# Performance work log

Hardware: AMD Instinct MI355X
Metric: run time of the kernel (lower is better)

Reference implementation:

```python
import jax, jax.numpy as jnp
import numpy as np

B, SQ, D = 4, 2048, 1536
HEADS, KV_HEADS, HEAD_DIM = 24, 12, 64
CROSS_DIM = 768
TEXT_LEN, NUM_TOKENS = 512, 64
ENC_LEN = TEXT_LEN + NUM_TOKENS
ROT_DIM = 32
IP_SCALE = 1.0
SCALE = 1.0 / np.sqrt(HEAD_DIM).astype(np.float32)


def _split_heads(x, n_heads):
    # [B, S, n_heads*HEAD_DIM] -> [B, n_heads, S, HEAD_DIM]
    b, s, _ = x.shape
    return x.reshape(b, s, n_heads, HEAD_DIM).transpose(0, 2, 1, 3)


def _repeat_kv(x):
    # [B, KV_HEADS, S, D] -> [B, HEADS, S, D] (repeat_interleave on head dim)
    return jnp.repeat(x, HEADS // KV_HEADS, axis=1)


def _apply_rope(x, cos, sin):
    # x: [B, H, S, ROT_DIM]; cos/sin: [S, ROT_DIM]; use_real_unbind_dim=-2 convention
    xr = x.reshape(*x.shape[:-1], 2, ROT_DIM // 2)
    x_real, x_imag = xr[..., 0, :], xr[..., 1, :]
    x_rot = jnp.concatenate([-x_imag, x_real], axis=-1)
    return x * cos[None, None] + x_rot * sin[None, None]


def _attn(q, k, v):
    scores = jnp.einsum('bhqd,bhkd->bhqk', q, k) * SCALE
    probs = jax.nn.softmax(scores.astype(jnp.float32), axis=-1).astype(q.dtype)
    return jnp.einsum('bhqk,bhkd->bhqd', probs, v)


def setup_inputs():
    key = jax.random.key(0)
    ks = jax.random.split(key, 10)
    t = jnp.arange(SQ, dtype=jnp.float32)
    freqs = 1.0 / (10000.0 ** (jnp.arange(ROT_DIM // 2, dtype=jnp.float32) / (ROT_DIM // 2)))
    ang = t[:, None] * freqs[None, :]  # [SQ, ROT_DIM//2]
    rope_cos = jnp.concatenate([jnp.cos(ang), jnp.cos(ang)], axis=-1)
    rope_sin = jnp.concatenate([jnp.sin(ang), jnp.sin(ang)], axis=-1)
    s = 0.02
    return {
        'hidden_states': jax.random.normal(ks[0], (B, SQ, D), jnp.float32),
        'encoder_hidden_states': jax.random.normal(ks[1], (B, ENC_LEN, CROSS_DIM), jnp.float32),
        'rope_cos': rope_cos,
        'rope_sin': rope_sin,
        'wq': jax.random.normal(ks[2], (D, HEADS * HEAD_DIM), jnp.float32) * s,
        'wk': jax.random.normal(ks[3], (CROSS_DIM, KV_HEADS * HEAD_DIM), jnp.float32) * s,
        'wv': jax.random.normal(ks[4], (CROSS_DIM, KV_HEADS * HEAD_DIM), jnp.float32) * s,
        'wk_ip': jax.random.normal(ks[5], (CROSS_DIM, KV_HEADS * HEAD_DIM), jnp.float32) * s,
        'wv_ip': jax.random.normal(ks[6], (CROSS_DIM, KV_HEADS * HEAD_DIM), jnp.float32) * s,
        'wo': jax.random.normal(ks[7], (HEADS * HEAD_DIM, D), jnp.float32) * s,
        'bo': jnp.zeros((D,), jnp.float32),
    }


def reference(hidden_states, encoder_hidden_states, rope_cos, rope_sin,
              wq, wk, wv, wk_ip, wv_ip, wo, bo):
    residual = hidden_states
    text = encoder_hidden_states[:, :TEXT_LEN, :]
    ip = encoder_hidden_states[:, TEXT_LEN:, :]

    q = _split_heads(hidden_states @ wq, HEADS)          # [B, H, SQ, Dh]
    k = _repeat_kv(_split_heads(text @ wk, KV_HEADS))    # [B, H, St, Dh]
    v = _repeat_kv(_split_heads(text @ wv, KV_HEADS))

    # RoPE in float32 on first ROT_DIM channels of Q only (cross-attention)
    q32 = q.astype(jnp.float32)
    q_rot = _apply_rope(q32[..., :ROT_DIM], rope_cos, rope_sin)
    q = jnp.concatenate([q_rot, q32[..., ROT_DIM:]], axis=-1).astype(hidden_states.dtype)

    out = _attn(q, k, v)                                 # [B, H, SQ, Dh]

    # IP-adapter branch
    ip_k = _repeat_kv(_split_heads(ip @ wk_ip, KV_HEADS))  # [B, H, NUM_TOKENS, Dh]
    ip_v = _repeat_kv(_split_heads(ip @ wv_ip, KV_HEADS))
    out = out + IP_SCALE * _attn(q, ip_k, ip_v)

    out = out.transpose(0, 2, 1, 3).reshape(B, SQ, HEADS * HEAD_DIM)
    out = out @ wo + bo
    return out + residual
```

## Files before the change

kernel.cpp:

```cpp
#include <hip/hip_runtime.h>
#include <hip/hip_bf16.h>

typedef __attribute__((ext_vector_type(8))) short short8;
typedef __attribute__((ext_vector_type(4))) short short4v;
typedef __attribute__((ext_vector_type(4))) float f32x4;

#define MFMA16(a, b, c) __builtin_amdgcn_mfma_f32_16x16x32_bf16(a, b, c, 0, 0, 0)
#define QK_SCALE_LOG2E 0.18033688011112042f

__device__ __forceinline__ short f2bf(float x) {
  union { float f; unsigned u; } v; v.f = x;
  unsigned u = v.u;
  u += 0x7FFFu + ((u >> 16) & 1u);
  return (short)(u >> 16);
}
__device__ __forceinline__ short f2bf_trunc(float x) {
  union { float f; unsigned u; } v; v.f = x;
  return (short)(v.u >> 16);
}

__device__ __forceinline__ void gload16(const void* g, void* l) {
  __builtin_amdgcn_global_load_lds(
      (const __attribute__((address_space(1))) unsigned int*)g,
      (__attribute__((address_space(3))) unsigned int*)l, 16, 0, 0);
}

__global__ __launch_bounds__(256) void conv_bf16_kernel(
    const float* __restrict__ in, short* __restrict__ out, int n4) {
  int i = blockIdx.x * 256 + threadIdx.x;
  if (i >= n4) return;
  f32x4 v = *(const f32x4*)(in + (size_t)i * 4);
  short4v s;
  s[0] = f2bf(v[0]); s[1] = f2bf(v[1]); s[2] = f2bf(v[2]); s[3] = f2bf(v[3]);
  *(short4v*)(out + (size_t)i * 4) = s;
}

__global__ __launch_bounds__(256) void enc_pack_kernel(
    const float* __restrict__ enc, short* __restrict__ text,
    short* __restrict__ ip) {
  int i4 = blockIdx.x * 256 + threadIdx.x;
  int i = i4 * 4;
  if (i >= 4 * 576 * 768) return;
  int c = i % 768;
  int rs = i / 768;
  int b = rs / 576, s = rs % 576;
  f32x4 v = *(const f32x4*)(enc + i);
  short4v o;
  o[0] = f2bf(v[0]); o[1] = f2bf(v[1]); o[2] = f2bf(v[2]); o[3] = f2bf(v[3]);
  if (s < 512)
    *(short4v*)(text + (size_t)(b * 512 + s) * 768 + c) = o;
  else
    *(short4v*)(ip + (size_t)(b * 64 + (s - 512)) * 768 + c) = o;
}

__global__ __launch_bounds__(256) void prep_weights_kernel(
    const float* __restrict__ wq, const float* __restrict__ wo,
    const float* __restrict__ wk, const float* __restrict__ wv,
    const float* __restrict__ wkip, const float* __restrict__ wvip,
    short* __restrict__ wqT, short* __restrict__ woT,
    short* __restrict__ wkvT, short* __restrict__ wkvipT) {
  __shared__ float tile[32][33];
  const int z = blockIdx.z;
  const float* src; short* dst; int N, row_off;
  if (z == 0)      { src = wq;   dst = wqT;    N = 1536; row_off = 0; }
  else if (z == 1) { src = wo;   dst = woT;    N = 1536; row_off = 0; }
  else if (z == 2) { src = wk;   dst = wkvT;   N = 768;  row_off = 0; }
  else if (z == 3) { src = wv;   dst = wkvT;   N = 768;  row_off = 768; }
  else if (z == 4) { src = wkip; dst = wkvipT; N = 768;  row_off = 0; }
  else             { src = wvip; dst = wkvipT; N = 768;  row_off = 768; }
  int c0 = blockIdx.x * 32, r0 = blockIdx.y * 32;
  if (c0 >= N || r0 >= N) return;
  int tx = threadIdx.x & 31, ty = threadIdx.x >> 5;
#pragma unroll
  for (int j = 0; j < 4; ++j)
    tile[ty + j * 8][tx] = src[(size_t)(r0 + ty + j * 8) * N + c0 + tx];
  __syncthreads();
#pragma unroll
  for (int j = 0; j < 4; ++j)
    dst[(size_t)(row_off + c0 + ty + j * 8) * N + r0 + tx] =
        f2bf(tile[tx][ty + j * 8]);
}

__device__ __forceinline__ void gemm_core(
    const short* __restrict__ A, const short* __restrict__ Bt, int K, int lda,
    int ldb, int row0, int col0, short* sA, short* sB, f32x4 acc[4][4]) {
  const int tid = threadIdx.x;
  const int lane = tid & 63;
  const int wid = tid >> 6;
  const int wr = (wid >> 1) * 64, wc = (wid & 1) * 64;
  const int lr = lane & 15;
  const int hk = (lane >> 4) * 16;
  const int xr = (lr & 7) << 4;

  for (int kt = 0; kt < K; kt += 64) {
#pragma unroll
    for (int q = 0; q < 4; ++q) {
      int L = q * 4096 + tid * 16;
      int r = L >> 7;
      int sb = (L & 127) ^ ((r & 7) << 4);
      int srcoff = kt + (sb >> 1);
      gload16(A + (size_t)(row0 + r) * lda + srcoff, (char*)sA + L);
      gload16(Bt + (size_t)(col0 + r) * ldb + srcoff, (char*)sB + L);
    }
    __syncthreads();
#pragma unroll
    for (int kk = 0; kk < 2; ++kk) {
      short8 af[4], bf[4];
#pragma unroll
      for (int m = 0; m < 4; ++m) {
        int row = wr + m * 16 + lr;
        af[m] = *(const short8*)((const char*)sA + row * 128 +
                                 ((kk * 64 + hk) ^ xr));
      }
#pragma unroll
      for (int n = 0; n < 4; ++n) {
        int row = wc + n * 16 + lr;
        bf[n] = *(const short8*)((const char*)sB + row * 128 +
                                 ((kk * 64 + hk) ^ xr));
      }
#pragma unroll
      for (int m = 0; m < 4; ++m)
#pragma unroll
        for (int n = 0; n < 4; ++n) acc[m][n] = MFMA16(af[m], bf[n], acc[m][n]);
    }
    __syncthreads();
  }
}

__device__ __forceinline__ void stage32(const short* __restrict__ gA,
                                        const short* __restrict__ gBt,
                                        int lda, int ldb, char* buf, int tid) {
#pragma unroll
  for (int li = 0; li < 2; ++li) {
    int L = li * 4096 + tid * 16;
    int row = L >> 6;
    int cb = (L & 63) ^ (((row >> 1) & 3) << 4);
    gload16(gA + (size_t)row * lda + (cb >> 1), buf + L);
    gload16(gBt + (size_t)row * ldb + (cb >> 1), buf + 8192 + L);
  }
}

template <int K>
__device__ __forceinline__ void gemm128p(
    const short* __restrict__ A, const short* __restrict__ Bt, int lda,
    int ldb, int row0, int col0, char* sm, f32x4 acc[4][4]) {
  const int tid = threadIdx.x;
  const int lane = tid & 63, wid = tid >> 6;
  const int wr = (wid >> 1) * 64, wc = (wid & 1) * 64;
  const int lr = lane & 15;
  const int hk = (lane >> 4) * 16;
  const int xr = ((lr >> 1) & 3) << 4;
  constexpr int NT = K / 32;

  const short* gA = A + (size_t)row0 * lda;
  const short* gB = Bt + (size_t)col0 * ldb;

  char* p0 = sm;
  char* p1 = sm + 16384;
  char* p2 = sm + 32768;

  stage32(gA, gB, lda, ldb, p0, tid);
  stage32(gA + 32, gB + 32, lda, ldb, p1, tid);
  asm volatile("s_waitcnt vmcnt(4)" ::: "memory");
  __builtin_amdgcn_s_barrier();

  for (int t = 0; t < NT; ++t) {
    if (t + 2 < NT)
      stage32(gA + (t + 2) * 32, gB + (t + 2) * 32, lda, ldb, p2, tid);
    __builtin_amdgcn_sched_barrier(0);
    short8 af[4], bf[4];
#pragma unroll
    for (int m = 0; m < 4; ++m) {
      int row = wr + m * 16 + lr;
      af[m] = *(const short8*)(p0 + row * 64 + (hk ^ xr));
    }
#pragma unroll
    for (int n = 0; n < 4; ++n) {
      int row = wc + n * 16 + lr;
      bf[n] = *(const short8*)(p0 + 8192 + row * 64 + (hk ^ xr));
    }
#pragma unroll
    for (int m = 0; m < 4; ++m)
#pragma unroll
      for (int n = 0; n < 4; ++n) acc[m][n] = MFMA16(af[m], bf[n], acc[m][n]);
    __builtin_amdgcn_sched_barrier(0);
    if (t + 2 < NT)
      asm volatile("s_waitcnt vmcnt(4)" ::: "memory");
    else
      asm volatile("s_waitcnt vmcnt(0)" ::: "memory");
    __builtin_amdgcn_s_barrier();
    char* tmp = p0; p0 = p1; p1 = p2; p2 = tmp;
  }
}

__device__ __forceinline__ void grid128(int& row0, int& col0) {
  int bid = blockIdx.x;
  int x = bid & 7;
  int j = bid >> 3;
  row0 = (x * 8 + (j & 7)) * 128;
  col0 = (j >> 3) * 128;
}

__global__ __launch_bounds__(256, 3) void q_proj_128p(
    const short* __restrict__ hsbf, const short* __restrict__ wqT,
    const float* __restrict__ rc, const float* __restrict__ rsn,
    short* __restrict__ qbuf) {
  __shared__ char sm[49152];
  f32x4 acc[4][4] = {};
  int row0, col0;
  grid128(row0, col0);
  gemm128p<1536>(hsbf, wqT, 1536, 1536, row0, col0, sm, acc);

  const int lane = threadIdx.x & 63, wid = threadIdx.x >> 6;
  const int wr = (wid >> 1) * 64, wc = (wid & 1) * 64;
  const int lr = lane & 15, lrow4 = (lane >> 4) * 4;
  const int h = (col0 + wc) >> 6;
#pragma unroll
  for (int m = 0; m < 4; ++m) {
#pragma unroll
    for (int r = 0; r < 4; ++r) {
      int grow = row0 + wr + m * 16 + lrow4 + r;
      int b = grow >> 11, t = grow & 2047;
      float v0 = acc[m][0][r], v1 = acc[m][1][r];
      float c0 = rc[t * 32 + lr], s0 = rsn[t * 32 + lr];
      float c1 = rc[t * 32 + 16 + lr], s1 = rsn[t * 32 + 16 + lr];
      float n0 = (v0 * c0 - v1 * s0) * QK_SCALE_LOG2E;
      float n1 = (v1 * c1 + v0 * s1) * QK_SCALE_LOG2E;
      short* ob = qbuf + ((size_t)(b * 24 + h) * 2048 + t) * 64;
      ob[lr] = f2bf(n0);
      ob[16 + lr] = f2bf(n1);
      ob[32 + lr] = f2bf(acc[m][2][r] * QK_SCALE_LOG2E);
      ob[48 + lr] = f2bf(acc[m][3][r] * QK_SCALE_LOG2E);
    }
  }
}

__global__ __launch_bounds__(256, 3) void o_proj_128p(
    const short* __restrict__ attnbf, const short* __restrict__ woT,
    const float* __restrict__ bo, const float* __restrict__ resid,
    float* __restrict__ out) {
  __shared__ char sm[49152];
  f32x4 acc[4][4] = {};
  int row0, col0;
  grid128(row0, col0);
  gemm128p<1536>(attnbf, woT, 1536, 1536, row0, col0, sm, acc);

  const int lane = threadIdx.x & 63, wid = threadIdx.x >> 6;
  const int wr = (wid >> 1) * 64, wc = (wid & 1) * 64;
  const int lr = lane & 15, lrow4 = (lane >> 4) * 4;
#pragma unroll
  for (int m = 0; m < 4; ++m) {
#pragma unroll
    for (int n = 0; n < 4; ++n) {
#pragma unroll
      for (int r = 0; r < 4; ++r) {
        int grow = row0 + wr + m * 16 + lrow4 + r;
        int gcol = col0 + wc + n * 16 + lr;
        size_t off = (size_t)grow * 1536 + gcol;
        out[off] = acc[m][n][r] + bo[gcol] + resid[off];
      }
    }
  }
}

__global__ __launch_bounds__(256) void kv_gemm(
    const short* __restrict__ Abf, const short* __restrict__ wkvT,
    short* __restrict__ kout, short* __restrict__ vtout, int rlog2) {
  __shared__ short sA[128 * 64];
  __shared__ short sB[128 * 64];
  f32x4 acc[4][4] = {};
  const int row0 = blockIdx.y * 128, col0 = blockIdx.x * 128;
  gemm_core(Abf, wkvT, 768, 768, 768, row0, col0, sA, sB, acc);

  const int tid = threadIdx.x;
  const int lane = tid & 63, wid = tid >> 6;
  const int wr = (wid >> 1) * 64, wc = (wid & 1) * 64;
  const int lr = lane & 15, lrow4 = (lane >> 4) * 4;
  const int rmask = (1 << rlog2) - 1;
#pragma unroll
  for (int m = 0; m < 4; ++m) {
#pragma unroll
    for (int n = 0; n < 4; ++n) {
#pragma unroll
      for (int r = 0; r < 4; ++r) {
        int grow = row0 + wr + m * 16 + lrow4 + r;
        int gcol = col0 + wc + n * 16 + lr;
        int b = grow >> rlog2, key = grow & rmask;
        short val = f2bf(acc[m][n][r]);
        if (gcol < 768) {
          int kvh = gcol >> 6, d = gcol & 63;
          kout[((((size_t)(b * 12 + kvh)) << rlog2) + key) * 64 + d] = val;
        } else {
          int c2 = gcol - 768;
          int kvh = c2 >> 6, d = c2 & 63;
          int kp = (key & ~31) | (((key >> 2) & 3) << 3) |
                   (((key >> 4) & 1) << 2) | (key & 3);
          vtout[(((size_t)((b * 12 + kvh) * 64 + d)) << rlog2) + kp] = val;
        }
      }
    }
  }
}

__device__ __forceinline__ void stage_tile(const short* __restrict__ ks,
                                           const short* __restrict__ vs,
                                           int vstr, short* kb, short* vb,
                                           int tid) {
#pragma unroll
  for (int q = 0; q < 2; ++q) {
    int L = q * 4096 + tid * 16;
    int row = L >> 7;
    int sc = ((L & 127) ^ ((row & 7) << 4)) >> 1;
    gload16(ks + row * 64 + sc, (char*)kb + L);
    gload16(vs + (size_t)row * vstr + sc, (char*)vb + L);
  }
}

__device__ __forceinline__ void attn_tile(const short* kb, const short* vb,
                                          const short8 qf[2],
                                          float& m_run, float& l_run,
                                          f32x4 o_acc[4], int lane) {
  const int lr = lane & 15, hi = lane >> 4;
  f32x4 s[4];
#pragma unroll
  for (int nf = 0; nf < 4; ++nf) {
    int row = nf * 16 + lr;
    int rx = (row & 7) << 4;
    const char* base = (const char*)kb + row * 128;
    short8 k0 = *(const short8*)(base + ((hi * 16) ^ rx));
    short8 k1 = *(const short8*)(base + ((64 + hi * 16) ^ rx));
    f32x4 a = {0.f, 0.f, 0.f, 0.f};
    a = MFMA16(k0, qf[0], a);
    a = MFMA16(k1, qf[1], a);
    s[nf] = a;
  }
  float mx = fmaxf(fmaxf(s[0][0], s[0][1]), fmaxf(s[0][2], s[0][3]));
#pragma unroll
  for (int nf = 1; nf < 4; ++nf)
    mx = fmaxf(mx, fmaxf(fmaxf(s[nf][0], s[nf][1]), fmaxf(s[nf][2], s[nf][3])));
  if (__any(mx - m_run > 8.0f)) {
    float mr = fmaxf(mx, __shfl_xor(mx, 16));
    mr = fmaxf(mr, __shfl_xor(mr, 32));
    float mn = fmaxf(m_run, mr);
    float corr = __builtin_amdgcn_exp2f(m_run - mn);
    m_run = mn;
    l_run *= corr;
#pragma unroll
    for (int r = 0; r < 4; ++r) {
      float cr = __shfl(corr, hi * 4 + r);
#pragma unroll
      for (int no = 0; no < 4; ++no) o_acc[no][r] *= cr;
    }
  }
  short8 pa[2];
#pragma unroll
  for (int nf = 0; nf < 4; ++nf) {
#pragma unroll
    for (int r = 0; r < 4; ++r) {
      float p = __builtin_amdgcn_exp2f(s[nf][r] - m_run);
      l_run += p;
      pa[nf >> 1][(nf & 1) * 4 + r] = f2bf_trunc(p);
    }
  }
#pragma unroll
  for (int ks = 0; ks < 2; ++ks) {
#pragma unroll
    for (int no = 0; no < 4; ++no) {
      int row = no * 16 + lr;
      int rx = (row & 7) << 4;
      short8 vf = *(const short8*)((const char*)vb + row * 128 +
                                   ((ks * 64 + hi * 16) ^ rx));
      o_acc[no] = MFMA16(pa[ks], vf, o_acc[no]);
    }
  }
}

__global__ __launch_bounds__(256, 4) void attn_kernel(
    const short* __restrict__ qbuf, const short* __restrict__ kbuf,
    const short* __restrict__ vtbuf, const short* __restrict__ kipbuf,
    const short* __restrict__ vtipbuf, short* __restrict__ attn_out) {
  const int tid = threadIdx.x;
  const int lane = tid & 63, wid = tid >> 6;
  const int f = (blockIdx.x & 7) * 384 + (blockIdx.x >> 3);
  const int qt = f & 31;
  const int h = (f >> 5) % 24;
  const int b = f / (32 * 24);
  const int kvh = h >> 1;
  const int lr = lane & 15, hi = lane >> 4;

  __shared__ short skv_k[2 * 64 * 64];
  __shared__ short skv_v[2 * 64 * 64];

  const short* qp = qbuf + (size_t)(b * 24 + h) * 2048 * 64;
  const short* kp = kbuf + (size_t)(b * 12 + kvh) * 512 * 64;
  const short* vp = vtbuf + (size_t)(b * 12 + kvh) * 64 * 512;
  const short* kip = kipbuf + (size_t)(b * 12 + kvh) * 64 * 64;
  const short* vip = vtipbuf + (size_t)(b * 12 + kvh) * 64 * 64;

  const int q0 = qt * 64 + wid * 16;
  short8 qf[2];
  qf[0] = *(const short8*)(qp + (size_t)(q0 + lr) * 64 + hi * 8);
  qf[1] = *(const short8*)(qp + (size_t)(q0 + lr) * 64 + 32 + hi * 8);

  float m1 = -1.0e30f, l1 = 0.f, m2 = -1.0e30f, l2 = 0.f;
  f32x4 oacc1[4] = {}, oacc2[4] = {};

  stage_tile(kp, vp, 512, skv_k, skv_v, tid);
  __syncthreads();

  for (int t = 0; t < 9; ++t) {
    int cur = t & 1, nxt = cur ^ 1;
    if (t < 8) {
      const short* ks_ = (t < 7) ? kp + (t + 1) * 64 * 64 : kip;
      const short* vs_ = (t < 7) ? vp + (t + 1) * 64 : vip;
      int vstr = (t < 7) ? 512 : 64;
      stage_tile(ks_, vs_, vstr, skv_k + nxt * 4096, skv_v + nxt * 4096, tid);
    }
    if (t < 8)
      attn_tile(skv_k + cur * 4096, skv_v + cur * 4096, qf, m1, l1, oacc1, lane);
    else
      attn_tile(skv_k + cur * 4096, skv_v + cur * 4096, qf, m2, l2, oacc2, lane);
    __syncthreads();
  }

  l1 += __shfl_xor(l1, 16); l1 += __shfl_xor(l1, 32);
  l2 += __shfl_xor(l2, 16); l2 += __shfl_xor(l2, 32);
  float inv1 = 1.0f / l1, inv2 = 1.0f / l2;
#pragma unroll
  for (int r = 0; r < 4; ++r) {
    float i1 = __shfl(inv1, hi * 4 + r);
    float i2 = __shfl(inv2, hi * 4 + r);
    int grow = b * 2048 + q0 + hi * 4 + r;
#pragma unroll
    for (int no = 0; no < 4; ++no) {
      float val = oacc1[no][r] * i1 + oacc2[no][r] * i2;
      attn_out[(size_t)grow * 1536 + h * 64 + no * 16 + lr] = f2bf(val);
    }
  }
}

extern "C" void kernel_launch(void* const* d_in, const int* in_sizes, int n_in,
                              void* d_out, int out_size, void* d_ws, size_t ws_size,
                              hipStream_t stream) {
  const float* hs = (const float*)d_in[0];
  const float* enc = (const float*)d_in[1];
  const float* rc = (const float*)d_in[2];
  const float* rsn = (const float*)d_in[3];
  const float* wq = (const float*)d_in[4];
  const float* wk = (const float*)d_in[5];
  const float* wv = (const float*)d_in[6];
  const float* wkip = (const float*)d_in[7];
  const float* wvip = (const float*)d_in[8];
  const float* wo = (const float*)d_in[9];
  const float* bo = (const float*)d_in[10];
  float* out = (float*)d_out;

  char* ws = (char*)d_ws;
  short* hsbf    = (short*)(ws + 0);
  short* attnbuf = (short*)(ws + 0);
  short* qbuf    = (short*)(ws + 25165824);
  short* kbuf    = (short*)(ws + 50331648);
  short* vtbuf   = (short*)(ws + 53477376);
  short* kipbuf  = (short*)(ws + 56623104);
  short* vtipbuf = (short*)(ws + 57016320);
  short* textbf  = (short*)(ws + 57409536);
  short* ipbf    = (short*)(ws + 60555264);
  short* wqT     = (short*)(ws + 60948480);
  short* woT     = (short*)(ws + 65667072);
  short* wkvT    = (short*)(ws + 70385664);
  short* wkvipT  = (short*)(ws + 72744960);

  conv_bf16_kernel<<<12288, 256, 0, stream>>>(hs, hsbf, 8192 * 1536 / 4);
  enc_pack_kernel<<<1728, 256, 0, stream>>>(enc, textbf, ipbf);
  prep_weights_kernel<<<dim3(48, 48, 6), 256, 0, stream>>>(
      wq, wo, wk, wv, wkip, wvip, wqT, woT, wkvT, wkvipT);

  q_proj_128p<<<768, 256, 0, stream>>>(hsbf, wqT, rc, rsn, qbuf);
  kv_gemm<<<dim3(12, 16), 256, 0, stream>>>(textbf, wkvT, kbuf, vtbuf, 9);
  kv_gemm<<<dim3(12, 2), 256, 0, stream>>>(ipbf, wkvipT, kipbuf, vtipbuf, 6);

  attn_kernel<<<3072, 256, 0, stream>>>(qbuf, kbuf, vtbuf, kipbuf,
                                        vtipbuf, attnbuf);

  o_proj_128p<<<768, 256, 0, stream>>>(attnbuf, woT, bo, hs, out);
}
```

Measured before the change: 218.8 us.

## Fuse fp32-to-bf16 conversion into Q projection and prefetch residual in O projection

The standalone conversion kernel for hidden_states is removed. The Q projection now loads fp32 rows into registers, converts them to bf16 and writes them into LDS inside its triple-buffered pipeline, which saves a full write and re-read of a 24MB bf16 copy. The O projection prefetches half of the residual tile during the last iterations to hide that load latency. kv_gemm is switched to the pipelined gemm128p path. The price is doubled A-side global traffic per tile (fp32), more VGPRs and hand-tuned waitcnt values that must match the load counts.

```diff
diff --git a/kernel.cpp b/kernel.cpp
--- a/kernel.cpp
+++ b/kernel.cpp
@@ -23,16 +23,6 @@
   __builtin_amdgcn_global_load_lds(
       (const __attribute__((address_space(1))) unsigned int*)g,
       (__attribute__((address_space(3))) unsigned int*)l, 16, 0, 0);
-}
-
-__global__ __launch_bounds__(256) void conv_bf16_kernel(
-    const float* __restrict__ in, short* __restrict__ out, int n4) {
-  int i = blockIdx.x * 256 + threadIdx.x;
-  if (i >= n4) return;
-  f32x4 v = *(const f32x4*)(in + (size_t)i * 4);
-  short4v s;
-  s[0] = f2bf(v[0]); s[1] = f2bf(v[1]); s[2] = f2bf(v[2]); s[3] = f2bf(v[3]);
-  *(short4v*)(out + (size_t)i * 4) = s;
 }
 
 __global__ __launch_bounds__(256) void enc_pack_kernel(
@@ -81,52 +71,6 @@
         f2bf(tile[tx][ty + j * 8]);
 }
 
-__device__ __forceinline__ void gemm_core(
-    const short* __restrict__ A, const short* __restrict__ Bt, int K, int lda,
-    int ldb, int row0, int col0, short* sA, short* sB, f32x4 acc[4][4]) {
-  const int tid = threadIdx.x;
-  const int lane = tid & 63;
-  const int wid = tid >> 6;
-  const int wr = (wid >> 1) * 64, wc = (wid & 1) * 64;
-  const int lr = lane & 15;
-  const int hk = (lane >> 4) * 16;
-  const int xr = (lr & 7) << 4;
-
-  for (int kt = 0; kt < K; kt += 64) {
-#pragma unroll
-    for (int q = 0; q < 4; ++q) {
-      int L = q * 4096 + tid * 16;
-      int r = L >> 7;
-      int sb = (L & 127) ^ ((r & 7) << 4);
-      int srcoff = kt + (sb >> 1);
-      gload16(A + (size_t)(row0 + r) * lda + srcoff, (char*)sA + L);
-      gload16(Bt + (size_t)(col0 + r) * ldb + srcoff, (char*)sB + L);
-    }
-    __syncthreads();
-#pragma unroll
-    for (int kk = 0; kk < 2; ++kk) {
-      short8 af[4], bf[4];
-#pragma unroll
-      for (int m = 0; m < 4; ++m) {
-        int row = wr + m * 16 + lr;
-        af[m] = *(const short8*)((const char*)sA + row * 128 +
-                                 ((kk * 64 + hk) ^ xr));
-      }
-#pragma unroll
-      for (int n = 0; n < 4; ++n) {
-        int row = wc + n * 16 + lr;
-        bf[n] = *(const short8*)((const char*)sB + row * 128 +
-                                 ((kk * 64 + hk) ^ xr));
-      }
-#pragma unroll
-      for (int m = 0; m < 4; ++m)
-#pragma unroll
-        for (int n = 0; n < 4; ++n) acc[m][n] = MFMA16(af[m], bf[n], acc[m][n]);
-    }
-    __syncthreads();
-  }
-}
-
 __device__ __forceinline__ void stage32(const short* __restrict__ gA,
                                         const short* __restrict__ gBt,
                                         int lda, int ldb, char* buf, int tid) {
@@ -138,6 +82,26 @@
     gload16(gA + (size_t)row * lda + (cb >> 1), buf + L);
     gload16(gBt + (size_t)row * ldb + (cb >> 1), buf + 8192 + L);
   }
+}
+
+__device__ __forceinline__ void compute32(const char* p0, int wr, int wc,
+                                          int lr, int hk, int xr,
+                                          f32x4 acc[4][4]) {
+  short8 af[4], bf[4];
+#pragma unroll
+  for (int m = 0; m < 4; ++m) {
+    int row = wr + m * 16 + lr;
+    af[m] = *(const short8*)(p0 + row * 64 + (hk ^ xr));
+  }
+#pragma unroll
+  for (int n = 0; n < 4; ++n) {
+    int row = wc + n * 16 + lr;
+    bf[n] = *(const short8*)(p0 + 8192 + row * 64 + (hk ^ xr));
+  }
+#pragma unroll
+  for (int m = 0; m < 4; ++m)
+#pragma unroll
+    for (int n = 0; n < 4; ++n) acc[m][n] = MFMA16(af[m], bf[n], acc[m][n]);
 }
 
 template <int K>
@@ -168,21 +132,7 @@
     if (t + 2 < NT)
       stage32(gA + (t + 2) * 32, gB + (t + 2) * 32, lda, ldb, p2, tid);
     __builtin_amdgcn_sched_barrier(0);
-    short8 af[4], bf[4];
-#pragma unroll
-    for (int m = 0; m < 4; ++m) {
-      int row = wr + m * 16 + lr;
-      af[m] = *(const short8*)(p0 + row * 64 + (hk ^ xr));
-    }
-#pragma unroll
-    for (int n = 0; n < 4; ++n) {
-      int row = wc + n * 16 + lr;
-      bf[n] = *(const short8*)(p0 + 8192 + row * 64 + (hk ^ xr));
-    }
-#pragma unroll
-    for (int m = 0; m < 4; ++m)
-#pragma unroll
-      for (int n = 0; n < 4; ++n) acc[m][n] = MFMA16(af[m], bf[n], acc[m][n]);
+    compute32(p0, wr, wc, lr, hk, xr, acc);
     __builtin_amdgcn_sched_barrier(0);
     if (t + 2 < NT)
       asm volatile("s_waitcnt vmcnt(4)" ::: "memory");
@@ -201,19 +151,98 @@
   col0 = (j >> 3) * 128;
 }
 
+__device__ __forceinline__ void q_issueA(const float* __restrict__ gAf,
+                                         int tid, f32x4 ar[4]) {
+#pragma unroll
+  for (int li = 0; li < 2; ++li) {
+    int L = li * 4096 + tid * 16;
+    int row = L >> 6;
+    int cb = (L & 63) ^ (((row >> 1) & 3) << 4);
+    const float* src = gAf + (size_t)row * 1536 + (cb >> 1);
+    ar[li * 2] = *(const f32x4*)src;
+    ar[li * 2 + 1] = *(const f32x4*)(src + 4);
+  }
+}
+__device__ __forceinline__ void q_writeA(char* buf, int tid, const f32x4 ar[4]) {
+#pragma unroll
+  for (int li = 0; li < 2; ++li) {
+    int L = li * 4096 + tid * 16;
+    short8 s;
+#pragma unroll
+    for (int j = 0; j < 4; ++j) {
+      s[j] = f2bf(ar[li * 2][j]);
+      s[j + 4] = f2bf(ar[li * 2 + 1][j]);
+    }
+    *(short8*)(buf + L) = s;
+  }
+}
+__device__ __forceinline__ void q_stageB(const short* __restrict__ gBt,
+                                         char* buf, int tid) {
+#pragma unroll
+  for (int li = 0; li < 2; ++li) {
+    int L = li * 4096 + tid * 16;
+    int row = L >> 6;
+    int cb = (L & 63) ^ (((row >> 1) & 3) << 4);
+    gload16(gBt + (size_t)row * 1536 + (cb >> 1), buf + 8192 + L);
+  }
+}
+
 __global__ __launch_bounds__(256, 3) void q_proj_128p(
-    const short* __restrict__ hsbf, const short* __restrict__ wqT,
+    const float* __restrict__ hs, const short* __restrict__ wqT,
     const float* __restrict__ rc, const float* __restrict__ rsn,
     short* __restrict__ qbuf) {
   __shared__ char sm[49152];
   f32x4 acc[4][4] = {};
   int row0, col0;
   grid128(row0, col0);
-  gemm128p<1536>(hsbf, wqT, 1536, 1536, row0, col0, sm, acc);
-
-  const int lane = threadIdx.x & 63, wid = threadIdx.x >> 6;
+
+  const int tid = threadIdx.x;
+  const int lane = tid & 63, wid = tid >> 6;
   const int wr = (wid >> 1) * 64, wc = (wid & 1) * 64;
-  const int lr = lane & 15, lrow4 = (lane >> 4) * 4;
+  const int lr = lane & 15;
+  const int hk = (lane >> 4) * 16;
+  const int xr = ((lr >> 1) & 3) << 4;
+  constexpr int NT = 48;
+
+  const float* gAf = hs + (size_t)row0 * 1536;
+  const short* gB = wqT + (size_t)col0 * 1536;
+  char* p0 = sm;
+  char* p1 = sm + 16384;
+  char* p2 = sm + 32768;
+  f32x4 arA[4], arB[4];
+
+  q_issueA(gAf, tid, arA);
+  q_stageB(gB, p0, tid);
+  q_issueA(gAf + 32, tid, arB);
+  q_stageB(gB + 32, p1, tid);
+  asm volatile("s_waitcnt vmcnt(8)" ::: "memory");
+  q_writeA(p0, tid, arA);
+  asm volatile("s_waitcnt vmcnt(6) lgkmcnt(0)" ::: "memory");
+  __builtin_amdgcn_s_barrier();
+
+  for (int t = 0; t < NT; ++t) {
+    if (t + 2 < NT) {
+      if ((t & 1) == 0) q_issueA(gAf + (t + 2) * 32, tid, arA);
+      else              q_issueA(gAf + (t + 2) * 32, tid, arB);
+      q_stageB(gB + (t + 2) * 32, p2, tid);
+    }
+    __builtin_amdgcn_sched_barrier(0);
+    compute32(p0, wr, wc, lr, hk, xr, acc);
+    __builtin_amdgcn_sched_barrier(0);
+    if (t + 2 < NT)
+      asm volatile("s_waitcnt vmcnt(2)" ::: "memory");
+    else
+      asm volatile("s_waitcnt vmcnt(0)" ::: "memory");
+    if (t + 1 < NT) {
+      if ((t & 1) == 0) q_writeA(p1, tid, arB);
+      else              q_writeA(p1, tid, arA);
+    }
+    asm volatile("s_waitcnt lgkmcnt(0)" ::: "memory");
+    __builtin_amdgcn_s_barrier();
+    char* tmp = p0; p0 = p1; p1 = p2; p2 = tmp;
+  }
+
+  const int lrow4 = (lane >> 4) * 4;
   const int h = (col0 + wc) >> 6;
 #pragma unroll
   for (int m = 0; m < 4; ++m) {
@@ -243,11 +272,52 @@
   f32x4 acc[4][4] = {};
   int row0, col0;
   grid128(row0, col0);
-  gemm128p<1536>(attnbf, woT, 1536, 1536, row0, col0, sm, acc);
-
-  const int lane = threadIdx.x & 63, wid = threadIdx.x >> 6;
+
+  const int tid = threadIdx.x;
+  const int lane = tid & 63, wid = tid >> 6;
   const int wr = (wid >> 1) * 64, wc = (wid & 1) * 64;
-  const int lr = lane & 15, lrow4 = (lane >> 4) * 4;
+  const int lr = lane & 15;
+  const int hk = (lane >> 4) * 16;
+  const int xr = ((lr >> 1) & 3) << 4;
+  const int lrow4 = (lane >> 4) * 4;
+  constexpr int NT = 48;
+
+  const short* gA = attnbf + (size_t)row0 * 1536;
+  const short* gB = woT + (size_t)col0 * 1536;
+  char* p0 = sm;
+  char* p1 = sm + 16384;
+  char* p2 = sm + 32768;
+  float rv[2][4][4];
+
+  stage32(gA, gB, 1536, 1536, p0, tid);
+  stage32(gA + 32, gB + 32, 1536, 1536, p1, tid);
+  asm volatile("s_waitcnt vmcnt(4)" ::: "memory");
+  __builtin_amdgcn_s_barrier();
+
+  for (int t = 0; t < NT; ++t) {
+    if (t + 2 < NT)
+      stage32(gA + (t + 2) * 32, gB + (t + 2) * 32, 1536, 1536, p2, tid);
+    if (t == NT - 2) {
+#pragma unroll
+      for (int m = 0; m < 2; ++m)
+#pragma unroll
+        for (int n = 0; n < 4; ++n)
+#pragma unroll
+          for (int r = 0; r < 4; ++r)
+            rv[m][n][r] = resid[(size_t)(row0 + wr + m * 16 + lrow4 + r) * 1536 +
+                                col0 + wc + n * 16 + lr];
+    }
+    __builtin_amdgcn_sched_barrier(0);
+    compute32(p0, wr, wc, lr, hk, xr, acc);
+    __builtin_amdgcn_sched_barrier(0);
+    if (t + 2 < NT)
+      asm volatile("s_waitcnt vmcnt(4)" ::: "memory");
+    else if (t == NT - 2)
+      asm volatile("s_waitcnt vmcnt(32)" ::: "memory");
+    __builtin_amdgcn_s_barrier();
+    char* tmp = p0; p0 = p1; p1 = p2; p2 = tmp;
+  }
+
 #pragma unroll
   for (int m = 0; m < 4; ++m) {
 #pragma unroll
@@ -257,20 +327,20 @@
         int grow = row0 + wr + m * 16 + lrow4 + r;
         int gcol = col0 + wc + n * 16 + lr;
         size_t off = (size_t)grow * 1536 + gcol;
-        out[off] = acc[m][n][r] + bo[gcol] + resid[off];
+        float rs = (m < 2) ? rv[m & 1][n][r] : resid[off];
+        out[off] = acc[m][n][r] + bo[gcol] + rs;
       }
     }
   }
 }
 
-__global__ __launch_bounds__(256) void kv_gemm(
+__global__ __launch_bounds__(256, 3) void kv_gemm(
     const short* __restrict__ Abf, const short* __restrict__ wkvT,
     short* __restrict__ kout, short* __restrict__ vtout, int rlog2) {
-  __shared__ short sA[128 * 64];
-  __shared__ short sB[128 * 64];
+  __shared__ char sm[49152];
   f32x4 acc[4][4] = {};
   const int row0 = blockIdx.y * 128, col0 = blockIdx.x * 128;
-  gemm_core(Abf, wkvT, 768, 768, 768, row0, col0, sA, sB, acc);
+  gemm128p<768>(Abf, wkvT, 768, 768, row0, col0, sm, acc);
 
   const int tid = threadIdx.x;
   const int lane = tid & 63, wid = tid >> 6;
@@ -456,7 +526,6 @@
   float* out = (float*)d_out;
 
   char* ws = (char*)d_ws;
-  short* hsbf    = (short*)(ws + 0);
   short* attnbuf = (short*)(ws + 0);
   short* qbuf    = (short*)(ws + 25165824);
   short* kbuf    = (short*)(ws + 50331648);
@@ -470,12 +539,11 @@
   short* wkvT    = (short*)(ws + 70385664);
   short* wkvipT  = (short*)(ws + 72744960);
 
-  conv_bf16_kernel<<<12288, 256, 0, stream>>>(hs, hsbf, 8192 * 1536 / 4);
   enc_pack_kernel<<<1728, 256, 0, stream>>>(enc, textbf, ipbf);
   prep_weights_kernel<<<dim3(48, 48, 6), 256, 0, stream>>>(
       wq, wo, wk, wv, wkip, wvip, wqT, woT, wkvT, wkvipT);
 
-  q_proj_128p<<<768, 256, 0, stream>>>(hsbf, wqT, rc, rsn, qbuf);
+  q_proj_128p<<<768, 256, 0, stream>>>(hs, wqT, rc, rsn, qbuf);
   kv_gemm<<<dim3(12, 16), 256, 0, stream>>>(textbf, wkvT, kbuf, vtbuf, 9);
   kv_gemm<<<dim3(12, 2), 256, 0, stream>>>(ipbf, wkvipT, kipbuf, vtipbuf, 6);
 
```

After: 229.4 us. +4.9%, slower.

## Use 256x256 ping-pong GEMM tiles for Q and O projections

Applied to the files above, without the earlier changes.

Replaces the 128x128 triple-buffered GEMM in the Q and output projections with a 256x256 tile run by 512-thread blocks. These use 128KB of dynamic LDS and an eight-phase schedule that interleaves half-tile staging with MFMA work under set priority. The goal is more data reuse per LDS byte and better overlap of global loads with matrix math. The KV projection also switches to the pipelined 128 GEMM. Grid size drops to 192 blocks, which risks underfilling 256 CUs and leaving a tail.

```diff
diff --git a/kernel.cpp b/kernel.cpp
--- a/kernel.cpp
+++ b/kernel.cpp
@@ -81,52 +81,6 @@
         f2bf(tile[tx][ty + j * 8]);
 }
 
-__device__ __forceinline__ void gemm_core(
-    const short* __restrict__ A, const short* __restrict__ Bt, int K, int lda,
-    int ldb, int row0, int col0, short* sA, short* sB, f32x4 acc[4][4]) {
-  const int tid = threadIdx.x;
-  const int lane = tid & 63;
-  const int wid = tid >> 6;
-  const int wr = (wid >> 1) * 64, wc = (wid & 1) * 64;
-  const int lr = lane & 15;
-  const int hk = (lane >> 4) * 16;
-  const int xr = (lr & 7) << 4;
-
-  for (int kt = 0; kt < K; kt += 64) {
-#pragma unroll
-    for (int q = 0; q < 4; ++q) {
-      int L = q * 4096 + tid * 16;
-      int r = L >> 7;
-      int sb = (L & 127) ^ ((r & 7) << 4);
-      int srcoff = kt + (sb >> 1);
-      gload16(A + (size_t)(row0 + r) * lda + srcoff, (char*)sA + L);
-      gload16(Bt + (size_t)(col0 + r) * ldb + srcoff, (char*)sB + L);
-    }
-    __syncthreads();
-#pragma unroll
-    for (int kk = 0; kk < 2; ++kk) {
-      short8 af[4], bf[4];
-#pragma unroll
-      for (int m = 0; m < 4; ++m) {
-        int row = wr + m * 16 + lr;
-        af[m] = *(const short8*)((const char*)sA + row * 128 +
-                                 ((kk * 64 + hk) ^ xr));
-      }
-#pragma unroll
-      for (int n = 0; n < 4; ++n) {
-        int row = wc + n * 16 + lr;
-        bf[n] = *(const short8*)((const char*)sB + row * 128 +
-                                 ((kk * 64 + hk) ^ xr));
-      }
-#pragma unroll
-      for (int m = 0; m < 4; ++m)
-#pragma unroll
-        for (int n = 0; n < 4; ++n) acc[m][n] = MFMA16(af[m], bf[n], acc[m][n]);
-    }
-    __syncthreads();
-  }
-}
-
 __device__ __forceinline__ void stage32(const short* __restrict__ gA,
                                         const short* __restrict__ gBt,
                                         int lda, int ldb, char* buf, int tid) {
@@ -138,6 +92,26 @@
     gload16(gA + (size_t)row * lda + (cb >> 1), buf + L);
     gload16(gBt + (size_t)row * ldb + (cb >> 1), buf + 8192 + L);
   }
+}
+
+__device__ __forceinline__ void compute32(const char* p0, int wr, int wc,
+                                          int lr, int hk, int xr,
+                                          f32x4 acc[4][4]) {
+  short8 af[4], bf[4];
+#pragma unroll
+  for (int m = 0; m < 4; ++m) {
+    int row = wr + m * 16 + lr;
+    af[m] = *(const short8*)(p0 + row * 64 + (hk ^ xr));
+  }
+#pragma unroll
+  for (int n = 0; n < 4; ++n) {
+    int row = wc + n * 16 + lr;
+    bf[n] = *(const short8*)(p0 + 8192 + row * 64 + (hk ^ xr));
+  }
+#pragma unroll
+  for (int m = 0; m < 4; ++m)
+#pragma unroll
+    for (int n = 0; n < 4; ++n) acc[m][n] = MFMA16(af[m], bf[n], acc[m][n]);
 }
 
 template <int K>
@@ -154,7 +128,6 @@
 
   const short* gA = A + (size_t)row0 * lda;
   const short* gB = Bt + (size_t)col0 * ldb;
-
   char* p0 = sm;
   char* p1 = sm + 16384;
   char* p2 = sm + 32768;
@@ -168,21 +141,7 @@
     if (t + 2 < NT)
       stage32(gA + (t + 2) * 32, gB + (t + 2) * 32, lda, ldb, p2, tid);
     __builtin_amdgcn_sched_barrier(0);
-    short8 af[4], bf[4];
-#pragma unroll
-    for (int m = 0; m < 4; ++m) {
-      int row = wr + m * 16 + lr;
-      af[m] = *(const short8*)(p0 + row * 64 + (hk ^ xr));
-    }
-#pragma unroll
-    for (int n = 0; n < 4; ++n) {
-      int row = wc + n * 16 + lr;
-      bf[n] = *(const short8*)(p0 + 8192 + row * 64 + (hk ^ xr));
-    }
-#pragma unroll
-    for (int m = 0; m < 4; ++m)
-#pragma unroll
-      for (int n = 0; n < 4; ++n) acc[m][n] = MFMA16(af[m], bf[n], acc[m][n]);
+    compute32(p0, wr, wc, lr, hk, xr, acc);
     __builtin_amdgcn_sched_barrier(0);
     if (t + 2 < NT)
       asm volatile("s_waitcnt vmcnt(4)" ::: "memory");
@@ -193,33 +152,150 @@
   }
 }
 
-__device__ __forceinline__ void grid128(int& row0, int& col0) {
+template <int KTOT>
+__device__ __forceinline__ void gemm256(
+    const short* __restrict__ A, const short* __restrict__ Bt, int lda,
+    int ldb, int row0, int col0, char* sm, f32x4 acc[8][4]) {
+  const int tid = threadIdx.x;
+  const int lane = tid & 63, wid = tid >> 6;
+  const int wgM = wid >> 2, wgN = wid & 3;
+  const int lr = lane & 15;
+  const int hk = (lane >> 4) * 16;
+  const int xr = (lr & 7) << 4;
+  constexpr int NT = KTOT / 64;
+  constexpr int NI = NT / 2;
+
+  const short* gA = A + (size_t)row0 * lda;
+  const short* gB = Bt + (size_t)col0 * ldb;
+
+  auto stgA = [&](int tile, int h) {
+#pragma unroll
+    for (int p = 0; p < 2; ++p) {
+      int L = p * 8192 + tid * 16;
+      int hi = L >> 7, c = L & 127;
+      int cb = c ^ ((hi & 7) << 4);
+      int r = ((hi >> 6) << 7) | (h << 6) | (hi & 63);
+      gload16(gA + (size_t)r * lda + tile * 64 + (cb >> 1),
+              sm + (tile & 1) * 32768 + h * 16384 + L);
+    }
+  };
+  auto stgB = [&](int tile, int h) {
+#pragma unroll
+    for (int p = 0; p < 2; ++p) {
+      int L = p * 8192 + tid * 16;
+      int hi = L >> 7, c = L & 127;
+      int cb = c ^ ((hi & 7) << 4);
+      int r = ((hi >> 5) << 6) | (h << 5) | (hi & 31);
+      gload16(gB + (size_t)r * ldb + tile * 64 + (cb >> 1),
+              sm + 65536 + (tile & 1) * 32768 + h * 16384 + L);
+    }
+  };
+
+  short8 bf[2][2];
+  auto loadA = [&](short8 af[4][2], int tile, int mh) {
+    const char* a = sm + (tile & 1) * 32768 + mh * 16384;
+#pragma unroll
+    for (int m = 0; m < 4; ++m) {
+      int hi = wgM * 64 + m * 16 + lr;
+#pragma unroll
+      for (int kk = 0; kk < 2; ++kk)
+        af[m][kk] = *(const short8*)(a + hi * 128 + ((kk * 64 + hk) ^ xr));
+    }
+  };
+  auto loadBf = [&](int tile, int nh) {
+    const char* b = sm + 65536 + (tile & 1) * 32768 + nh * 16384;
+#pragma unroll
+    for (int n = 0; n < 2; ++n) {
+      int hi = wgN * 32 + n * 16 + lr;
+#pragma unroll
+      for (int kk = 0; kk < 2; ++kk)
+        bf[n][kk] = *(const short8*)(b + hi * 128 + ((kk * 64 + hk) ^ xr));
+    }
+  };
+  auto mmac = [&](short8 af[4][2], int mh, int nh) {
+    __builtin_amdgcn_s_setprio(1);
+#pragma unroll
+    for (int m = 0; m < 4; ++m)
+#pragma unroll
+      for (int n = 0; n < 2; ++n) {
+        acc[mh * 4 + m][nh * 2 + n] =
+            MFMA16(af[m][0], bf[n][0], acc[mh * 4 + m][nh * 2 + n]);
+        acc[mh * 4 + m][nh * 2 + n] =
+            MFMA16(af[m][1], bf[n][1], acc[mh * 4 + m][nh * 2 + n]);
+      }
+    __builtin_amdgcn_s_setprio(0);
+  };
+
+#define PH_SYNC()                                         \
+  __builtin_amdgcn_s_barrier();                           \
+  asm volatile("s_waitcnt lgkmcnt(0)" ::: "memory");      \
+  __builtin_amdgcn_sched_barrier(0)
+#define PH_END()                                          \
+  __builtin_amdgcn_sched_barrier(0);                      \
+  __builtin_amdgcn_s_barrier()
+
+  stgB(0, 0); stgA(0, 0); stgA(0, 1); stgB(0, 1);
+  stgB(1, 0); stgA(1, 0);
+  asm volatile("s_waitcnt vmcnt(4)" ::: "memory");
+  __builtin_amdgcn_s_barrier();
+
+  for (int i = 0; i < NI; ++i) {
+    const int u = 2 * i, v = 2 * i + 1, w = 2 * i + 2, x = 2 * i + 3;
+    const bool sg = (i + 1 < NI);
+    { short8 af[4][2]; loadA(af, u, 0); loadBf(u, 0); stgA(v, 1);
+      PH_SYNC(); mmac(af, 0, 0); PH_END(); }
+    { short8 af[4][2]; loadA(af, u, 1); stgB(v, 1);
+      PH_SYNC(); mmac(af, 1, 0); PH_END(); }
+    { short8 af[4][2]; loadA(af, u, 0); loadBf(u, 1); if (sg) stgB(w, 0);
+      PH_SYNC(); mmac(af, 0, 1); PH_END(); }
+    { short8 af[4][2]; loadA(af, u, 1); if (sg) stgA(w, 0);
+      PH_SYNC(); mmac(af, 1, 1);
+      __builtin_amdgcn_sched_barrier(0);
+      if (sg) asm volatile("s_waitcnt vmcnt(4)" ::: "memory");
+      else    asm volatile("s_waitcnt vmcnt(0)" ::: "memory");
+      PH_END(); }
+    { short8 af[4][2]; loadA(af, v, 0); loadBf(v, 0); if (sg) stgA(w, 1);
+      PH_SYNC(); mmac(af, 0, 0); PH_END(); }
+    { short8 af[4][2]; loadA(af, v, 1); if (sg) stgB(w, 1);
+      PH_SYNC(); mmac(af, 1, 0); PH_END(); }
+    { short8 af[4][2]; loadA(af, v, 0); loadBf(v, 1); if (sg) stgB(x, 0);
+      PH_SYNC(); mmac(af, 0, 1); PH_END(); }
+    { short8 af[4][2]; loadA(af, v, 1); if (sg) stgA(x, 0);
+      PH_SYNC(); mmac(af, 1, 1);
+      __builtin_amdgcn_sched_barrier(0);
+      if (sg) asm volatile("s_waitcnt vmcnt(4)" ::: "memory");
+      PH_END(); }
+  }
+#undef PH_SYNC
+#undef PH_END
+}
+
+__device__ __forceinline__ void grid256(int& row0, int& col0) {
   int bid = blockIdx.x;
-  int x = bid & 7;
-  int j = bid >> 3;
-  row0 = (x * 8 + (j & 7)) * 128;
-  col0 = (j >> 3) * 128;
-}
-
-__global__ __launch_bounds__(256, 3) void q_proj_128p(
+  int x = bid & 7, j = bid >> 3;
+  row0 = (x * 4 + (j & 3)) * 256;
+  col0 = (j >> 2) * 256;
+}
+
+__global__ __launch_bounds__(512, 2) void q_proj_256(
     const short* __restrict__ hsbf, const short* __restrict__ wqT,
     const float* __restrict__ rc, const float* __restrict__ rsn,
     short* __restrict__ qbuf) {
-  __shared__ char sm[49152];
-  f32x4 acc[4][4] = {};
+  extern __shared__ char sm[];
+  f32x4 acc[8][4] = {};
   int row0, col0;
-  grid128(row0, col0);
-  gemm128p<1536>(hsbf, wqT, 1536, 1536, row0, col0, sm, acc);
+  grid256(row0, col0);
+  gemm256<1536>(hsbf, wqT, 1536, 1536, row0, col0, sm, acc);
 
   const int lane = threadIdx.x & 63, wid = threadIdx.x >> 6;
-  const int wr = (wid >> 1) * 64, wc = (wid & 1) * 64;
+  const int wgM = wid >> 2, wgN = wid & 3;
   const int lr = lane & 15, lrow4 = (lane >> 4) * 4;
-  const int h = (col0 + wc) >> 6;
-#pragma unroll
-  for (int m = 0; m < 4; ++m) {
+  const int h = (col0 + wgN * 64) >> 6;
+#pragma unroll
+  for (int m = 0; m < 8; ++m) {
 #pragma unroll
     for (int r = 0; r < 4; ++r) {
-      int grow = row0 + wr + m * 16 + lrow4 + r;
+      int grow = row0 + wgM * 128 + m * 16 + lrow4 + r;
       int b = grow >> 11, t = grow & 2047;
       float v0 = acc[m][0][r], v1 = acc[m][1][r];
       float c0 = rc[t * 32 + lr], s0 = rsn[t * 32 + lr];
@@ -235,27 +311,27 @@
   }
 }
 
-__global__ __launch_bounds__(256, 3) void o_proj_128p(
+__global__ __launch_bounds__(512, 2) void o_proj_256(
     const short* __restrict__ attnbf, const short* __restrict__ woT,
     const float* __restrict__ bo, const float* __restrict__ resid,
     float* __restrict__ out) {
-  __shared__ char sm[49152];
-  f32x4 acc[4][4] = {};
+  extern __shared__ char sm[];
+  f32x4 acc[8][4] = {};
   int row0, col0;
-  grid128(row0, col0);
-  gemm128p<1536>(attnbf, woT, 1536, 1536, row0, col0, sm, acc);
+  grid256(row0, col0);
+  gemm256<1536>(attnbf, woT, 1536, 1536, row0, col0, sm, acc);
 
   const int lane = threadIdx.x & 63, wid = threadIdx.x >> 6;
-  const int wr = (wid >> 1) * 64, wc = (wid & 1) * 64;
+  const int wgM = wid >> 2, wgN = wid & 3;
   const int lr = lane & 15, lrow4 = (lane >> 4) * 4;
 #pragma unroll
-  for (int m = 0; m < 4; ++m) {
+  for (int m = 0; m < 8; ++m) {
 #pragma unroll
     for (int n = 0; n < 4; ++n) {
 #pragma unroll
       for (int r = 0; r < 4; ++r) {
-        int grow = row0 + wr + m * 16 + lrow4 + r;
-        int gcol = col0 + wc + n * 16 + lr;
+        int grow = row0 + wgM * 128 + m * 16 + lrow4 + r;
+        int gcol = col0 + wgN * 64 + n * 16 + lr;
         size_t off = (size_t)grow * 1536 + gcol;
         out[off] = acc[m][n][r] + bo[gcol] + resid[off];
       }
@@ -263,14 +339,13 @@
   }
 }
 
-__global__ __launch_bounds__(256) void kv_gemm(
+__global__ __launch_bounds__(256, 3) void kv_gemm(
     const short* __restrict__ Abf, const short* __restrict__ wkvT,
     short* __restrict__ kout, short* __restrict__ vtout, int rlog2) {
-  __shared__ short sA[128 * 64];
-  __shared__ short sB[128 * 64];
+  __shared__ char sm[49152];
   f32x4 acc[4][4] = {};
   const int row0 = blockIdx.y * 128, col0 = blockIdx.x * 128;
-  gemm_core(Abf, wkvT, 768, 768, 768, row0, col0, sA, sB, acc);
+  gemm128p<768>(Abf, wkvT, 768, 768, row0, col0, sm, acc);
 
   const int tid = threadIdx.x;
   const int lane = tid & 63, wid = tid >> 6;
@@ -470,17 +545,22 @@
   short* wkvT    = (short*)(ws + 70385664);
   short* wkvipT  = (short*)(ws + 72744960);
 
+  hipFuncSetAttribute((const void*)q_proj_256,
+                      hipFuncAttributeMaxDynamicSharedMemorySize, 131072);
+  hipFuncSetAttribute((const void*)o_proj_256,
+                      hipFuncAttributeMaxDynamicSharedMemorySize, 131072);
+
   conv_bf16_kernel<<<12288, 256, 0, stream>>>(hs, hsbf, 8192 * 1536 / 4);
   enc_pack_kernel<<<1728, 256, 0, stream>>>(enc, textbf, ipbf);
   prep_weights_kernel<<<dim3(48, 48, 6), 256, 0, stream>>>(
       wq, wo, wk, wv, wkip, wvip, wqT, woT, wkvT, wkvipT);
 
-  q_proj_128p<<<768, 256, 0, stream>>>(hsbf, wqT, rc, rsn, qbuf);
+  q_proj_256<<<192, 512, 131072, stream>>>(hsbf, wqT, rc, rsn, qbuf);
   kv_gemm<<<dim3(12, 16), 256, 0, stream>>>(textbf, wkvT, kbuf, vtbuf, 9);
   kv_gemm<<<dim3(12, 2), 256, 0, stream>>>(ipbf, wkvipT, kipbuf, vtipbuf, 6);
 
   attn_kernel<<<3072, 256, 0, stream>>>(qbuf, kbuf, vtbuf, kipbuf,
                                         vtipbuf, attnbuf);
 
-  o_proj_128p<<<768, 256, 0, stream>>>(attnbuf, woT, bo, hs, out);
-}
+  o_proj_256<<<192, 512, 131072, stream>>>(attnbuf, woT, bo, hs, out);
+}
```

Measured after the change: 209.2 us. 1.05x faster.
